# Kernel tuning notes

Hardware: AMD Instinct MI355X
Metric: run time of the kernel (lower is better)

## Reference

```python
import jax, jax.numpy as jnp
import numpy as np


def _squash(s, axis=-1, eps=1e-8):
    # squash(s) = |s|^2/(1+|s|^2) * s/|s|
    s2 = jnp.sum(s * s, axis=axis, keepdims=True)
    return (s2 / (1.0 + s2)) * s / jnp.sqrt(s2 + eps)


def _conv(x, w, b, stride):
    y = jax.lax.conv_general_dilated(
        x, w, (stride, stride), 'VALID',
        dimension_numbers=('NCHW', 'OIHW', 'NCHW'))
    return y + b[None, :, None, None]


def setup_inputs() -> dict:
    key = jax.random.key(0)
    ks = jax.random.split(key, 4)
    B = 64
    sc = 0.05
    return {
        'x': jax.random.normal(ks[0], (B, 3, 32, 32), jnp.float32),
        'conv_w': jax.random.normal(ks[1], (256, 3, 9, 9), jnp.float32) * sc,
        'conv_b': jnp.zeros((256,), jnp.float32),
        'pcap_w': jax.random.normal(ks[2], (256, 256, 9, 9), jnp.float32) * sc,
        'pcap_b': jnp.zeros((256,), jnp.float32),
        'W': jax.random.normal(ks[3], (100, 2048, 16, 8), jnp.float32) * sc,
    }


def reference(x, conv_w, conv_b, pcap_w, pcap_b, W):
    # Conv stem: [B,3,32,32] -> [B,256,24,24]
    h = jax.nn.relu(_conv(x, conv_w, conv_b, 1))
    # PrimaryCaps conv: [B,256,24,24] -> [B,256,8,8], then view to capsules
    p = _conv(h, pcap_w, pcap_b, 2)
    u = _squash(p.reshape(p.shape[0], 2048, 8))            # [B,2048,8]
    # DenseCapsule: u_hat[b,o,i,d] = W[o,i,d,k] u[b,i,k]
    u_hat = jnp.einsum('oidk,bik->boid', W, u)             # [B,100,2048,16]
    u_hat_sg = jax.lax.stop_gradient(u_hat)
    b = jnp.zeros(u_hat.shape[:3], u_hat.dtype)            # [B,100,2048]
    routings = 3
    v = None
    for i in range(routings):
        c = jax.nn.softmax(b, axis=1)                      # over out caps
        uh = u_hat if i == routings - 1 else u_hat_sg
        v = _squash(jnp.einsum('boi,boid->bod', c, uh))    # [B,100,16]
        if i < routings - 1:
            b = b + jnp.einsum('bod,boid->boi', v, u_hat_sg)
    return v
```

## Files before the change

### kernel.cpp

```cpp
#include <hip/hip_runtime.h>

#define NB 64
#define NO 100
#define NI 2048
#define ND 16
#define NK 8

#define WS_H    0
#define WS_U    9437184
#define WS_BB   10485760
#define WS_CB   23592960
#define WS_SP   36700160
#define WS_V    38338560
#define WS_PP   WS_BB

typedef __attribute__((ext_vector_type(8))) short bf16x8;
typedef __attribute__((ext_vector_type(16))) float f32x16;
typedef __attribute__((ext_vector_type(4))) float f32x4;

__device__ inline unsigned short f2bf(float x) {
    union { float f; unsigned u; } v; v.f = x;
    unsigned r = (v.u + 0x7FFFu + ((v.u >> 16) & 1u)) >> 16;
    return (unsigned short)r;
}
__device__ inline float bf2f(unsigned short h) {
    union { unsigned u; float f; } v; v.u = ((unsigned)h) << 16;
    return v.f;
}

__global__ __launch_bounds__(256) void conv1_kernel(const float* __restrict__ x,
        const float* __restrict__ w, const float* __restrict__ bias,
        unsigned short* __restrict__ h_hi, unsigned short* __restrict__ h_lo) {
    const int b = blockIdx.x;
    const int ocg = blockIdx.y;
    __shared__ float xl[3 * 32 * 32];
    __shared__ float wl[16 * 243];
    const int tid = threadIdx.x;
    for (int idx = tid; idx < 3072; idx += 256) xl[idx] = x[b * 3072 + idx];
    for (int idx = tid; idx < 16 * 243; idx += 256)
        wl[idx] = w[ocg * 16 * 243 + idx];
    __syncthreads();
    const int lane = tid & 63;
    const int wg = tid >> 6;
    float acc[4][9];
    #pragma unroll
    for (int jj = 0; jj < 4; ++jj) {
        float bv = bias[ocg * 16 + wg * 4 + jj];
        #pragma unroll
        for (int j = 0; j < 9; ++j) acc[jj][j] = bv;
    }
    int xbase[9];
    #pragma unroll
    for (int j = 0; j < 9; ++j) {
        int p = lane + 64 * j;
        xbase[j] = (p / 24) * 32 + (p % 24);
    }
    for (int ic = 0; ic < 3; ++ic)
        for (int ky = 0; ky < 9; ++ky) {
            #pragma unroll
            for (int kx = 0; kx < 9; ++kx) {
                float wv[4];
                #pragma unroll
                for (int jj = 0; jj < 4; ++jj)
                    wv[jj] = wl[(wg * 4 + jj) * 243 + ic * 81 + ky * 9 + kx];
                #pragma unroll
                for (int j = 0; j < 9; ++j) {
                    float xv = xl[ic * 1024 + xbase[j] + ky * 32 + kx];
                    #pragma unroll
                    for (int jj = 0; jj < 4; ++jj)
                        acc[jj][j] = fmaf(xv, wv[jj], acc[jj][j]);
                }
            }
        }
    #pragma unroll
    for (int jj = 0; jj < 4; ++jj) {
        int oc = ocg * 16 + wg * 4 + jj;
        #pragma unroll
        for (int j = 0; j < 9; ++j) {
            int p = lane + 64 * j;
            float v = fmaxf(acc[jj][j], 0.f);
            unsigned short hi = f2bf(v);
            unsigned short lo = f2bf(v - bf2f(hi));
            size_t o = (size_t)(b * 256 + oc) * 576 + p;
            h_hi[o] = hi;
            h_lo[o] = lo;
        }
    }
}

__global__ __launch_bounds__(256) void wb_precompute_kernel(const float* __restrict__ w,
        unsigned short* __restrict__ wBhi, unsigned short* __restrict__ wBlo) {
    const int ic = blockIdx.x;
    const int ocq = blockIdx.y;
    __shared__ float tl[64][85];
    const int tid = threadIdx.x;
    for (int f = tid; f < 5184; f += 256) {
        int oc = f / 81, kk = f % 81;
        tl[oc][kk] = w[(size_t)(ocq * 64 + oc) * 20736 + ic * 81 + kk];
    }
    __syncthreads();
    for (int idx = tid; idx < 9216; idx += 256) {
        int ky = idx >> 10;
        int rem = idx & 1023;
        int ocl = rem >> 4;
        int kx = rem & 15;
        float val = (kx < 9) ? tl[ocl][ky * 9 + kx] : 0.f;
        unsigned short hi = f2bf(val);
        unsigned short lo = f2bf(val - bf2f(hi));
        size_t dst = ((size_t)(ic * 9 + ky) * 256 + ocq * 64 + ocl) * 16 + kx;
        wBhi[dst] = hi;
        wBlo[dst] = lo;
    }
}

__global__ __launch_bounds__(256) void conv2_mfma_kernel(
        const unsigned short* __restrict__ h_hi, const unsigned short* __restrict__ h_lo,
        const unsigned short* __restrict__ wBhi, const unsigned short* __restrict__ wBlo,
        float* __restrict__ pp) {
    const int bpair = blockIdx.x;
    const int ocb = blockIdx.y;
    const int ks = blockIdx.z;
    __shared__ __align__(16) unsigned short Bh[2][128 * 16];
    __shared__ __align__(16) unsigned short Bl[2][128 * 16];
    const int tid = threadIdx.x;
    const int lane = tid & 63;
    const int wid = tid >> 6;
    const int wr = wid >> 1, wc = wid & 1;
    const int l31 = lane & 31, kh = lane >> 5;
    const int slot = tid & 127;
    const int role = tid >> 7;
    const int oy = (slot >> 3) & 7;
    const int ox = slot & 7;
    const unsigned short* hsel = role ? h_lo : h_hi;
    const size_t hrow0 = ((size_t)(bpair * 2 + (slot >> 6)) * 256) * 576;
    const int ic0 = ks * 32;

    const int aoff0 = (wr * 64 + l31) * 16 + kh * 8;
    const int aoff1 = aoff0 + 512;
    const int boff0 = (wc * 64 + l31) * 16 + kh * 8;
    const int boff1 = boff0 + 512;

    f32x16 acc[2][2];
    #pragma unroll
    for (int m = 0; m < 2; ++m)
        #pragma unroll
        for (int n = 0; n < 2; ++n)
            #pragma unroll
            for (int r = 0; r < 16; ++r) acc[m][n][r] = 0.f;

    unsigned int d0, d1, d2, d3, d4;

#define GLOADB(c) { const int ic_ = ic0 + (c) / 9, ky_ = (c) % 9;                          \
    const unsigned int* hp_ = (const unsigned int*)(hsel + hrow0 + (size_t)ic_ * 576       \
        + (2 * oy + ky_) * 24 + 2 * ox);                                                   \
    d0 = hp_[0]; d1 = hp_[1]; d2 = hp_[2]; d3 = hp_[3]; d4 = hp_[4]; }
#define STOREB(buf) { unsigned short* Bdst_ = (role ? Bl[buf] : Bh[buf]) + slot * 16;      \
    uint4 w0_; w0_.x = d0; w0_.y = d1; w0_.z = d2; w0_.w = d3;                             \
    uint4 w1_; w1_.x = d4 & 0xFFFFu; w1_.y = 0u; w1_.z = 0u; w1_.w = 0u;                   \
    *(uint4*)Bdst_ = w0_; *(uint4*)(Bdst_ + 8) = w1_; }
#define LOADA(c, AH, AL) { const int ic_ = ic0 + (c) / 9, ky_ = (c) % 9;                   \
    const size_t base_ = (size_t)ic_ * 36864 + (size_t)ky_ * 4096 + ocb * 2048;            \
    AH[0] = *(const bf16x8*)(wBhi + base_ + aoff0);                                        \
    AH[1] = *(const bf16x8*)(wBhi + base_ + aoff1);                                        \
    AL[0] = *(const bf16x8*)(wBlo + base_ + aoff0);                                        \
    AL[1] = *(const bf16x8*)(wBlo + base_ + aoff1); }
#define MFMA12(AH, AL, buf) {                                                              \
    bf16x8 bh0 = *(const bf16x8*)&Bh[buf][boff0];                                          \
    bf16x8 bh1 = *(const bf16x8*)&Bh[buf][boff1];                                          \
    bf16x8 bl0 = *(const bf16x8*)&Bl[buf][boff0];                                          \
    bf16x8 bl1 = *(const bf16x8*)&Bl[buf][boff1];                                          \
    acc[0][0] = __builtin_amdgcn_mfma_f32_32x32x16_bf16(AH[0], bh0, acc[0][0], 0, 0, 0);   \
    acc[0][0] = __builtin_amdgcn_mfma_f32_32x32x16_bf16(AH[0], bl0, acc[0][0], 0, 0, 0);   \
    acc[0][0] = __builtin_amdgcn_mfma_f32_32x32x16_bf16(AL[0], bh0, acc[0][0], 0, 0, 0);   \
    acc[0][1] = __builtin_amdgcn_mfma_f32_32x32x16_bf16(AH[0], bh1, acc[0][1], 0, 0, 0);   \
    acc[0][1] = __builtin_amdgcn_mfma_f32_32x32x16_bf16(AH[0], bl1, acc[0][1], 0, 0, 0);   \
    acc[0][1] = __builtin_amdgcn_mfma_f32_32x32x16_bf16(AL[0], bh1, acc[0][1], 0, 0, 0);   \
    acc[1][0] = __builtin_amdgcn_mfma_f32_32x32x16_bf16(AH[1], bh0, acc[1][0], 0, 0, 0);   \
    acc[1][0] = __builtin_amdgcn_mfma_f32_32x32x16_bf16(AH[1], bl0, acc[1][0], 0, 0, 0);   \
    acc[1][0] = __builtin_amdgcn_mfma_f32_32x32x16_bf16(AL[1], bh0, acc[1][0], 0, 0, 0);   \
    acc[1][1] = __builtin_amdgcn_mfma_f32_32x32x16_bf16(AH[1], bh1, acc[1][1], 0, 0, 0);   \
    acc[1][1] = __builtin_amdgcn_mfma_f32_32x32x16_bf16(AH[1], bl1, acc[1][1], 0, 0, 0);   \
    acc[1][1] = __builtin_amdgcn_mfma_f32_32x32x16_bf16(AL[1], bh1, acc[1][1], 0, 0, 0); }

    bf16x8 a0h[2], a0l[2], a1h[2], a1l[2];
    GLOADB(0); STOREB(0);
    GLOADB(1);
    LOADA(0, a0h, a0l);
    __syncthreads();
    #pragma unroll 1
    for (int c = 0; c < 288; c += 2) {
        LOADA(c + 1, a1h, a1l);
        MFMA12(a0h, a0l, 0);
        STOREB(1);
        if (c + 2 < 288) GLOADB(c + 2);
        __syncthreads();
        if (c + 2 < 288) LOADA(c + 2, a0h, a0l);
        MFMA12(a1h, a1l, 1);
        if (c + 2 < 288) {
            STOREB(0);
            GLOADB(c + 3);
        }
        __syncthreads();
    }
#undef GLOADB
#undef STOREB
#undef LOADA
#undef MFMA12

    const int b = bpair * 2 + ((wc * 64 + l31) >> 6);
    #pragma unroll
    for (int m = 0; m < 2; ++m)
        #pragma unroll
        for (int n = 0; n < 2; ++n) {
            const int slotg = wc * 64 + n * 32 + l31;
            const int bb = bpair * 2 + (slotg >> 6);
            const int pos = slotg & 63;
            #pragma unroll
            for (int r = 0; r < 16; ++r) {
                const int row = (r & 3) + 8 * (r >> 2) + 4 * kh;
                const int oc = ocb * 128 + wr * 64 + m * 32 + row;
                pp[(((size_t)ks * 64 + bb) * 256 + oc) * 64 + pos] = acc[m][n][r];
            }
        }
    (void)b;
}

__global__ __launch_bounds__(256) void reduce_bias_squash_kernel(
        const float* __restrict__ pp, const float* __restrict__ bias,
        float* __restrict__ u) {
    const int cap = blockIdx.x * 256 + threadIdx.x;
    const int b = cap >> 11;
    const int rem = cap & 2047;
    const int oc = rem >> 3;
    const int oy = rem & 7;
    float4 sa = {0.f, 0.f, 0.f, 0.f}, sb = {0.f, 0.f, 0.f, 0.f};
    #pragma unroll
    for (int ks = 0; ks < 8; ++ks) {
        const float4* p4 = (const float4*)&pp[(((size_t)ks * 64 + b) * 256 + oc) * 64 + oy * 8];
        float4 a = p4[0], c = p4[1];
        sa.x += a.x; sa.y += a.y; sa.z += a.z; sa.w += a.w;
        sb.x += c.x; sb.y += c.y; sb.z += c.z; sb.w += c.w;
    }
    const float bv = bias[oc];
    sa.x += bv; sa.y += bv; sa.z += bv; sa.w += bv;
    sb.x += bv; sb.y += bv; sb.z += bv; sb.w += bv;
    float s2 = sa.x * sa.x + sa.y * sa.y + sa.z * sa.z + sa.w * sa.w
             + sb.x * sb.x + sb.y * sb.y + sb.z * sb.z + sb.w * sb.w;
    float scale = (s2 / (1.f + s2)) / sqrtf(s2 + 1e-8f);
    sa.x *= scale; sa.y *= scale; sa.z *= scale; sa.w *= scale;
    sb.x *= scale; sb.y *= scale; sb.z *= scale; sb.w *= scale;
    float4* up = (float4*)&u[(size_t)cap * 8];
    up[0] = sa;
    up[1] = sb;
}

__global__ __launch_bounds__(256) void transpose_u_kernel(const float* __restrict__ u,
        float* __restrict__ ut) {
    const int blk = blockIdx.x;
    __shared__ float tl[64 * 132];
    const int tid = threadIdx.x;
    #pragma unroll
    for (int rep = 0; rep < 8; ++rep) {
        const int idx = tid + 256 * rep;
        const int b = idx >> 5, q = idx & 31;
        float4 uv = *(const float4*)(u + (size_t)b * 16384 + blk * 128 + 4 * q);
        *(float4*)&tl[b * 132 + 4 * q] = uv;
    }
    __syncthreads();
    #pragma unroll
    for (int rep = 0; rep < 32; ++rep) {
        const int row = rep * 4 + (tid >> 6);
        const int b = tid & 63;
        ut[(size_t)(blk * 128 + row) * 64 + b] = tl[b * 132 + row];
    }
}

template <int UNIFORM>
__global__ __launch_bounds__(256) void r_weighted_mfma_kernel(
        const float* __restrict__ W, const float* __restrict__ u,
        const float* __restrict__ cbuf, float* __restrict__ sp) {
    const int o = blockIdx.x;
    const int st = blockIdx.y;
    __shared__ __align__(16) unsigned short Ahi[16 * 72];
    __shared__ __align__(16) unsigned short Alo[16 * 72];
    __shared__ __align__(16) unsigned short Bhi[64 * 72];
    __shared__ __align__(16) unsigned short Blo[64 * 72];
    const int tid = threadIdx.x;
    const int lane = tid & 63;
    const int w = tid >> 6;
    const int l15 = lane & 15;
    const int hi = lane >> 4;
    const int sb = tid >> 2;
    const int si = tid & 3;
    f32x4 acc = {0.f, 0.f, 0.f, 0.f};
    const float* Wo = W + (size_t)o * 262144;
    const int i_base = st * 256;
    #pragma unroll 1
    for (int iter = 0; iter < 32; ++iter) {
        const int i0 = i_base + iter * 8;
        __syncthreads();
        {
            float4 wv = *(const float4*)(Wo + (size_t)i0 * 128 + 4 * tid);
            const int i_l = tid >> 5;
            const int d = (tid >> 1) & 15;
            const int k0 = (tid & 1) * 4;
            unsigned short* dh = Ahi + d * 72 + i_l * 8 + k0;
            unsigned short* dl = Alo + d * 72 + i_l * 8 + k0;
            float vv[4] = {wv.x, wv.y, wv.z, wv.w};
            unsigned int h01, h23, l01, l23;
            unsigned short h, l;
            h = f2bf(vv[0]); l = f2bf(vv[0] - bf2f(h)); h01 = h; l01 = l;
            h = f2bf(vv[1]); l = f2bf(vv[1] - bf2f(h)); h01 |= (unsigned)h << 16; l01 |= (unsigned)l << 16;
            h = f2bf(vv[2]); l = f2bf(vv[2] - bf2f(h)); h23 = h; l23 = l;
            h = f2bf(vv[3]); l = f2bf(vv[3] - bf2f(h)); h23 |= (unsigned)h << 16; l23 |= (unsigned)l << 16;
            *(unsigned int*)dh = h01; *(unsigned int*)(dh + 2) = h23;
            *(unsigned int*)dl = l01; *(unsigned int*)(dl + 2) = l23;
        }
        #pragma unroll
        for (int half = 0; half < 2; ++half) {
            const int i_l = si + 4 * half;
            const float* up = u + (size_t)sb * 16384 + (size_t)(i0 + i_l) * 8;
            float4 u0 = *(const float4*)up;
            float4 u1 = *(const float4*)(up + 4);
            float cv = UNIFORM ? 0.01f
                               : cbuf[(size_t)sb * (NO * NI) + o * NI + i0 + i_l];
            float q[8] = {u0.x * cv, u0.y * cv, u0.z * cv, u0.w * cv,
                          u1.x * cv, u1.y * cv, u1.z * cv, u1.w * cv};
            uint4 ph, pl;
            unsigned short h0, h1, l0, l1;
            h0 = f2bf(q[0]); l0 = f2bf(q[0] - bf2f(h0));
            h1 = f2bf(q[1]); l1 = f2bf(q[1] - bf2f(h1));
            ph.x = h0 | ((unsigned)h1 << 16); pl.x = l0 | ((unsigned)l1 << 16);
            h0 = f2bf(q[2]); l0 = f2bf(q[2] - bf2f(h0));
            h1 = f2bf(q[3]); l1 = f2bf(q[3] - bf2f(h1));
            ph.y = h0 | ((unsigned)h1 << 16); pl.y = l0 | ((unsigned)l1 << 16);
            h0 = f2bf(q[4]); l0 = f2bf(q[4] - bf2f(h0));
            h1 = f2bf(q[5]); l1 = f2bf(q[5] - bf2f(h1));
            ph.z = h0 | ((unsigned)h1 << 16); pl.z = l0 | ((unsigned)l1 << 16);
            h0 = f2bf(q[6]); l0 = f2bf(q[6] - bf2f(h0));
            h1 = f2bf(q[7]); l1 = f2bf(q[7] - bf2f(h1));
            ph.w = h0 | ((unsigned)h1 << 16); pl.w = l0 | ((unsigned)l1 << 16);
            *(uint4*)(Bhi + sb * 72 + i_l * 8) = ph;
            *(uint4*)(Blo + sb * 72 + i_l * 8) = pl;
        }
        __syncthreads();
        #pragma unroll
        for (int ch = 0; ch < 2; ++ch) {
            bf16x8 ah = *(const bf16x8*)(Ahi + l15 * 72 + ch * 32 + hi * 8);
            bf16x8 al = *(const bf16x8*)(Alo + l15 * 72 + ch * 32 + hi * 8);
            bf16x8 bh = *(const bf16x8*)(Bhi + (w * 16 + l15) * 72 + ch * 32 + hi * 8);
            bf16x8 bl = *(const bf16x8*)(Blo + (w * 16 + l15) * 72 + ch * 32 + hi * 8);
            acc = __builtin_amdgcn_mfma_f32_16x16x32_bf16(ah, bh, acc, 0, 0, 0);
            acc = __builtin_amdgcn_mfma_f32_16x16x32_bf16(ah, bl, acc, 0, 0, 0);
            acc = __builtin_amdgcn_mfma_f32_16x16x32_bf16(al, bh, acc, 0, 0, 0);
        }
    }
    const int bg = w * 16 + l15;
    float4 st4;
    st4.x = acc[0]; st4.y = acc[1]; st4.z = acc[2]; st4.w = acc[3];
    *(float4*)&sp[(((size_t)o * 8 + st) * 64 + bg) * 16 + hi * 4] = st4;
}

__global__ __launch_bounds__(256) void squash_v_kernel(const float* __restrict__ sp,
        float* __restrict__ dest) {
    const int t = blockIdx.x * 256 + threadIdx.x;
    const int d = t & 15;
    const int cap = t >> 4;
    const int o = cap >> 6;
    const int bb = cap & 63;
    float s = 0.f;
    #pragma unroll
    for (int st = 0; st < 8; ++st)
        s += sp[(((size_t)o * 8 + st) * 64 + bb) * 16 + d];
    float s2 = s * s;
    #pragma unroll
    for (int off = 1; off < 16; off <<= 1)
        s2 += __shfl_xor(s2, off, 16);
    float scale = (s2 / (1.f + s2)) / sqrtf(s2 + 1e-8f);
    dest[(bb * NO + o) * ND + d] = s * scale;
}

template <int ADD>
__global__ __launch_bounds__(256) void r_logits_mfma_kernel(
        const float* __restrict__ W, const float* __restrict__ ut,
        const float* __restrict__ v, float* __restrict__ bbuf) {
    const int o = blockIdx.x;
    const int st = blockIdx.y;
    __shared__ __align__(16) unsigned short Aext[128 * 40];
    __shared__ __align__(16) unsigned short B1[64 * 40];
    __shared__ __align__(16) unsigned short B2[64 * 40];
    __shared__ float ul[128 * 66];
    const int tid = threadIdx.x;
    const int lane = tid & 63;
    const int w = tid >> 6;
    const int l15 = lane & 15;
    const int hi = lane >> 4;
    const float* Wo = W + (size_t)o * 262144;
    {
        const int b = tid >> 2;
        const int dq = (tid & 3) * 4;
        float4 vv = *(const float4*)&v[((size_t)b * NO + o) * ND + dq];
        float q[4] = {vv.x, vv.y, vv.z, vv.w};
        #pragma unroll
        for (int c = 0; c < 4; ++c) {
            unsigned short h = f2bf(q[c]);
            unsigned short l = f2bf(q[c] - bf2f(h));
            B1[b * 40 + dq + c] = h;
            B1[b * 40 + 16 + dq + c] = h;
            B2[b * 40 + dq + c] = l;
            B2[b * 40 + 16 + dq + c] = 0;
        }
    }
    __syncthreads();
    #pragma unroll 1
    for (int iter = 0; iter < 8; ++iter) {
        __syncthreads();
        #pragma unroll
        for (int rep = 0; rep < 2; ++rep) {
            const int off = 4 * tid + 1024 * rep;
            float4 wv = *(const float4*)(Wo + (size_t)(st * 128 + iter * 16) * 128 + off);
            const int i_l = off >> 7;
            const int d = (off >> 3) & 15;
            const int k0 = off & 7;
            float va[4] = {wv.x, wv.y, wv.z, wv.w};
            #pragma unroll
            for (int c = 0; c < 4; ++c) {
                unsigned short h = f2bf(va[c]);
                unsigned short l = f2bf(va[c] - bf2f(h));
                const int row = i_l * 8 + k0 + c;
                Aext[row * 40 + d] = h;
                Aext[row * 40 + 16 + d] = l;
            }
        }
        const int base_row = (st * 128 + iter * 16) * 8;
        #pragma unroll
        for (int rep = 0; rep < 8; ++rep) {
            const int idx = tid + 256 * rep;
            const int row = idx >> 4, bq = idx & 15;
            float4 uv = *(const float4*)(ut + (size_t)(base_row + row) * 64 + 4 * bq);
            *(float4*)&ul[row * 66 + 4 * bq] = uv;
        }
        __syncthreads();
        f32x4 acc[8];
        bf16x8 bf1 = *(const bf16x8*)&B1[(w * 16 + l15) * 40 + hi * 8];
        bf16x8 bf2 = *(const bf16x8*)&B2[(w * 16 + l15) * 40 + hi * 8];
        #pragma unroll
        for (int mt = 0; mt < 8; ++mt) {
            f32x4 z = {0.f, 0.f, 0.f, 0.f};
            bf16x8 af = *(const bf16x8*)&Aext[(mt * 16 + l15) * 40 + hi * 8];
            z = __builtin_amdgcn_mfma_f32_16x16x32_bf16(af, bf1, z, 0, 0, 0);
            z = __builtin_amdgcn_mfma_f32_16x16x32_bf16(af, bf2, z, 0, 0, 0);
            acc[mt] = z;
        }
        #pragma unroll
        for (int mt = 0; mt < 8; ++mt) {
            float partial = 0.f;
            #pragma unroll
            for (int r = 0; r < 4; ++r) {
                const int grow = mt * 16 + hi * 4 + r;
                partial = fmaf(acc[mt][r], ul[grow * 66 + w * 16 + l15], partial);
            }
            float sum = partial + __shfl_xor(partial, 16);
            if ((hi & 1) == 0) {
                const int i_glob = st * 128 + iter * 16 + mt * 2 + (hi >> 1);
                const int bg = w * 16 + l15;
                const size_t addr = (size_t)bg * (NO * NI) + (size_t)o * NI + i_glob;
                bbuf[addr] = (ADD ? bbuf[addr] : 0.f) + sum;
            }
        }
    }
}

__global__ __launch_bounds__(256) void softmax_kernel(const float* __restrict__ bbuf,
        float* __restrict__ cbuf) {
    const int bb = blockIdx.x >> 3;
    const int i = (blockIdx.x & 7) * 256 + threadIdx.x;
    const float* col = bbuf + bb * (NO * NI) + i;
    float m = -1e30f;
    for (int o = 0; o < NO; ++o) m = fmaxf(m, col[o * NI]);
    float s = 0.f;
    for (int o = 0; o < NO; ++o) s += __expf(col[o * NI] - m);
    const float inv = 1.f / s;
    float* outp = cbuf + bb * (NO * NI) + i;
    for (int o = 0; o < NO; ++o) outp[o * NI] = __expf(col[o * NI] - m) * inv;
}

extern "C" void kernel_launch(void* const* d_in, const int* in_sizes, int n_in,
                              void* d_out, int out_size, void* d_ws, size_t ws_size,
                              hipStream_t stream) {
    (void)in_sizes; (void)n_in; (void)out_size; (void)ws_size;
    const float* x      = (const float*)d_in[0];
    const float* conv_w = (const float*)d_in[1];
    const float* conv_b = (const float*)d_in[2];
    const float* pcap_w = (const float*)d_in[3];
    const float* pcap_b = (const float*)d_in[4];
    const float* W      = (const float*)d_in[5];
    float* out = (float*)d_out;
    float* ws  = (float*)d_ws;
    unsigned short* h_hi = (unsigned short*)(ws + WS_H);
    unsigned short* h_lo = h_hi + 9437184;
    unsigned short* wBhi = (unsigned short*)(ws + WS_CB);
    unsigned short* wBlo = wBhi + 9437184;
    float* ut  = ws + WS_H;
    float* u   = ws + WS_U;
    float* bbf = ws + WS_BB;
    float* cbf = ws + WS_CB;
    float* sp  = ws + WS_SP;
    float* v   = ws + WS_V;
    float* pp  = ws + WS_PP;

    wb_precompute_kernel<<<dim3(256, 4), 256, 0, stream>>>(pcap_w, wBhi, wBlo);
    conv1_kernel<<<dim3(64, 16), 256, 0, stream>>>(x, conv_w, conv_b, h_hi, h_lo);
    conv2_mfma_kernel<<<dim3(32, 2, 8), 256, 0, stream>>>(h_hi, h_lo, wBhi, wBlo, pp);
    reduce_bias_squash_kernel<<<512, 256, 0, stream>>>(pp, pcap_b, u);
    transpose_u_kernel<<<128, 256, 0, stream>>>(u, ut);
    r_weighted_mfma_kernel<1><<<dim3(100, 8), 256, 0, stream>>>(W, u, nullptr, sp);
    squash_v_kernel<<<400, 256, 0, stream>>>(sp, v);
    r_logits_mfma_kernel<0><<<dim3(100, 16), 256, 0, stream>>>(W, ut, v, bbf);
    softmax_kernel<<<512, 256, 0, stream>>>(bbf, cbf);
    r_weighted_mfma_kernel<0><<<dim3(100, 8), 256, 0, stream>>>(W, u, cbf, sp);
    squash_v_kernel<<<400, 256, 0, stream>>>(sp, v);
    r_logits_mfma_kernel<1><<<dim3(100, 16), 256, 0, stream>>>(W, ut, v, bbf);
    softmax_kernel<<<512, 256, 0, stream>>>(bbf, cbf);
    r_weighted_mfma_kernel<0><<<dim3(100, 8), 256, 0, stream>>>(W, u, cbf, sp);
    squash_v_kernel<<<400, 256, 0, stream>>>(sp, out);
}
```

Baseline: 850.8 us.

## Pad conv2 LDS B tile rows and simplify double-buffer pipeline

Pads each B-tile row in shared memory from 16 to 20 bf16 elements to reduce LDS bank conflicts on the MFMA operand reads, switching the reads and writes to 8-byte accesses. The main loop also becomes a single-step double buffer: the next global B load is issued, the A weights for the current step are loaded directly, and then the MFMAs run. This removes the A-register prefetch one step ahead, so weight-load latency may be less hidden, and narrower LDS accesses add instruction count.

```diff
diff --git a/kernel.cpp b/kernel.cpp
--- a/kernel.cpp
+++ b/kernel.cpp
@@ -120,8 +120,8 @@
     const int bpair = blockIdx.x;
     const int ocb = blockIdx.y;
     const int ks = blockIdx.z;
-    __shared__ __align__(16) unsigned short Bh[2][128 * 16];
-    __shared__ __align__(16) unsigned short Bl[2][128 * 16];
+    __shared__ __align__(16) unsigned short Bh[2][128 * 20];
+    __shared__ __align__(16) unsigned short Bl[2][128 * 20];
     const int tid = threadIdx.x;
     const int lane = tid & 63;
     const int wid = tid >> 6;
@@ -134,11 +134,9 @@
     const unsigned short* hsel = role ? h_lo : h_hi;
     const size_t hrow0 = ((size_t)(bpair * 2 + (slot >> 6)) * 256) * 576;
     const int ic0 = ks * 32;
-
-    const int aoff0 = (wr * 64 + l31) * 16 + kh * 8;
-    const int aoff1 = aoff0 + 512;
-    const int boff0 = (wc * 64 + l31) * 16 + kh * 8;
-    const int boff1 = boff0 + 512;
+    const size_t abase = (size_t)ocb * 2048 + (size_t)(wr * 64 + l31) * 16 + kh * 8;
+    const int boff0 = (wc * 64 + l31) * 20 + kh * 8;
+    const int boff1 = boff0 + 32 * 20;
 
     f32x16 acc[2][2];
     #pragma unroll
@@ -149,65 +147,63 @@
             for (int r = 0; r < 16; ++r) acc[m][n][r] = 0.f;
 
     unsigned int d0, d1, d2, d3, d4;
+    bf16x8 ah0, ah1, al0, al1;
 
 #define GLOADB(c) { const int ic_ = ic0 + (c) / 9, ky_ = (c) % 9;                          \
     const unsigned int* hp_ = (const unsigned int*)(hsel + hrow0 + (size_t)ic_ * 576       \
         + (2 * oy + ky_) * 24 + 2 * ox);                                                   \
     d0 = hp_[0]; d1 = hp_[1]; d2 = hp_[2]; d3 = hp_[3]; d4 = hp_[4]; }
-#define STOREB(buf) { unsigned short* Bdst_ = (role ? Bl[buf] : Bh[buf]) + slot * 16;      \
-    uint4 w0_; w0_.x = d0; w0_.y = d1; w0_.z = d2; w0_.w = d3;                             \
-    uint4 w1_; w1_.x = d4 & 0xFFFFu; w1_.y = 0u; w1_.z = 0u; w1_.w = 0u;                   \
-    *(uint4*)Bdst_ = w0_; *(uint4*)(Bdst_ + 8) = w1_; }
-#define LOADA(c, AH, AL) { const int ic_ = ic0 + (c) / 9, ky_ = (c) % 9;                   \
-    const size_t base_ = (size_t)ic_ * 36864 + (size_t)ky_ * 4096 + ocb * 2048;            \
-    AH[0] = *(const bf16x8*)(wBhi + base_ + aoff0);                                        \
-    AH[1] = *(const bf16x8*)(wBhi + base_ + aoff1);                                        \
-    AL[0] = *(const bf16x8*)(wBlo + base_ + aoff0);                                        \
-    AL[1] = *(const bf16x8*)(wBlo + base_ + aoff1); }
-#define MFMA12(AH, AL, buf) {                                                              \
-    bf16x8 bh0 = *(const bf16x8*)&Bh[buf][boff0];                                          \
-    bf16x8 bh1 = *(const bf16x8*)&Bh[buf][boff1];                                          \
-    bf16x8 bl0 = *(const bf16x8*)&Bl[buf][boff0];                                          \
-    bf16x8 bl1 = *(const bf16x8*)&Bl[buf][boff1];                                          \
-    acc[0][0] = __builtin_amdgcn_mfma_f32_32x32x16_bf16(AH[0], bh0, acc[0][0], 0, 0, 0);   \
-    acc[0][0] = __builtin_amdgcn_mfma_f32_32x32x16_bf16(AH[0], bl0, acc[0][0], 0, 0, 0);   \
-    acc[0][0] = __builtin_amdgcn_mfma_f32_32x32x16_bf16(AL[0], bh0, acc[0][0], 0, 0, 0);   \
-    acc[0][1] = __builtin_amdgcn_mfma_f32_32x32x16_bf16(AH[0], bh1, acc[0][1], 0, 0, 0);   \
-    acc[0][1] = __builtin_amdgcn_mfma_f32_32x32x16_bf16(AH[0], bl1, acc[0][1], 0, 0, 0);   \
-    acc[0][1] = __builtin_amdgcn_mfma_f32_32x32x16_bf16(AL[0], bh1, acc[0][1], 0, 0, 0);   \
-    acc[1][0] = __builtin_amdgcn_mfma_f32_32x32x16_bf16(AH[1], bh0, acc[1][0], 0, 0, 0);   \
-    acc[1][0] = __builtin_amdgcn_mfma_f32_32x32x16_bf16(AH[1], bl0, acc[1][0], 0, 0, 0);   \
-    acc[1][0] = __builtin_amdgcn_mfma_f32_32x32x16_bf16(AL[1], bh0, acc[1][0], 0, 0, 0);   \
-    acc[1][1] = __builtin_amdgcn_mfma_f32_32x32x16_bf16(AH[1], bh1, acc[1][1], 0, 0, 0);   \
-    acc[1][1] = __builtin_amdgcn_mfma_f32_32x32x16_bf16(AH[1], bl1, acc[1][1], 0, 0, 0);   \
-    acc[1][1] = __builtin_amdgcn_mfma_f32_32x32x16_bf16(AL[1], bh1, acc[1][1], 0, 0, 0); }
-
-    bf16x8 a0h[2], a0l[2], a1h[2], a1l[2];
-    GLOADB(0); STOREB(0);
-    GLOADB(1);
-    LOADA(0, a0h, a0l);
+#define STOREB(buf) { unsigned short* Bdst_ = (role ? Bl[buf] : Bh[buf]) + slot * 20;      \
+    uint2 p0_; p0_.x = d0; p0_.y = d1;                                                     \
+    uint2 p1_; p1_.x = d2; p1_.y = d3;                                                     \
+    uint2 p2_; p2_.x = d4 & 0xFFFFu; p2_.y = 0u;                                           \
+    uint2 p3_; p3_.x = 0u; p3_.y = 0u;                                                     \
+    *(uint2*)(Bdst_) = p0_; *(uint2*)(Bdst_ + 4) = p1_;                                    \
+    *(uint2*)(Bdst_ + 8) = p2_; *(uint2*)(Bdst_ + 12) = p3_; }
+#define LOADA(c) { const int ic_ = ic0 + (c) / 9, ky_ = (c) % 9;                           \
+    const size_t base_ = (size_t)ic_ * 36864 + (size_t)ky_ * 4096 + abase;                 \
+    ah0 = *(const bf16x8*)(wBhi + base_);                                                  \
+    ah1 = *(const bf16x8*)(wBhi + base_ + 512);                                            \
+    al0 = *(const bf16x8*)(wBlo + base_);                                                  \
+    al1 = *(const bf16x8*)(wBlo + base_ + 512); }
+#define LDSB(arr, off, dst) { union { struct { uint2 a, b; } p; bf16x8 v; } u_;            \
+    u_.p.a = *(const uint2*)((arr) + (off));                                               \
+    u_.p.b = *(const uint2*)((arr) + (off) + 4);                                           \
+    dst = u_.v; }
+#define MFMA12(buf) { bf16x8 bh0, bh1, bl0, bl1;                                           \
+    LDSB(Bh[buf], boff0, bh0); LDSB(Bh[buf], boff1, bh1);                                  \
+    LDSB(Bl[buf], boff0, bl0); LDSB(Bl[buf], boff1, bl1);                                  \
+    acc[0][0] = __builtin_amdgcn_mfma_f32_32x32x16_bf16(ah0, bh0, acc[0][0], 0, 0, 0);     \
+    acc[0][0] = __builtin_amdgcn_mfma_f32_32x32x16_bf16(ah0, bl0, acc[0][0], 0, 0, 0);     \
+    acc[0][0] = __builtin_amdgcn_mfma_f32_32x32x16_bf16(al0, bh0, acc[0][0], 0, 0, 0);     \
+    acc[0][1] = __builtin_amdgcn_mfma_f32_32x32x16_bf16(ah0, bh1, acc[0][1], 0, 0, 0);     \
+    acc[0][1] = __builtin_amdgcn_mfma_f32_32x32x16_bf16(ah0, bl1, acc[0][1], 0, 0, 0);     \
+    acc[0][1] = __builtin_amdgcn_mfma_f32_32x32x16_bf16(al0, bh1, acc[0][1], 0, 0, 0);     \
+    acc[1][0] = __builtin_amdgcn_mfma_f32_32x32x16_bf16(ah1, bh0, acc[1][0], 0, 0, 0);     \
+    acc[1][0] = __builtin_amdgcn_mfma_f32_32x32x16_bf16(ah1, bl0, acc[1][0], 0, 0, 0);     \
+    acc[1][0] = __builtin_amdgcn_mfma_f32_32x32x16_bf16(al1, bh0, acc[1][0], 0, 0, 0);     \
+    acc[1][1] = __builtin_amdgcn_mfma_f32_32x32x16_bf16(ah1, bh1, acc[1][1], 0, 0, 0);     \
+    acc[1][1] = __builtin_amdgcn_mfma_f32_32x32x16_bf16(ah1, bl1, acc[1][1], 0, 0, 0);     \
+    acc[1][1] = __builtin_amdgcn_mfma_f32_32x32x16_bf16(al1, bh1, acc[1][1], 0, 0, 0); }
+
+    GLOADB(0);
+    STOREB(0);
     __syncthreads();
     #pragma unroll 1
-    for (int c = 0; c < 288; c += 2) {
-        LOADA(c + 1, a1h, a1l);
-        MFMA12(a0h, a0l, 0);
-        STOREB(1);
-        if (c + 2 < 288) GLOADB(c + 2);
-        __syncthreads();
-        if (c + 2 < 288) LOADA(c + 2, a0h, a0l);
-        MFMA12(a1h, a1l, 1);
-        if (c + 2 < 288) {
-            STOREB(0);
-            GLOADB(c + 3);
-        }
+    for (int c = 0; c < 288; ++c) {
+        const int cur = c & 1;
+        if (c < 287) GLOADB(c + 1);
+        LOADA(c);
+        MFMA12(cur);
+        if (c < 287) STOREB(cur ^ 1);
         __syncthreads();
     }
 #undef GLOADB
 #undef STOREB
 #undef LOADA
+#undef LDSB
 #undef MFMA12
 
-    const int b = bpair * 2 + ((wc * 64 + l31) >> 6);
     #pragma unroll
     for (int m = 0; m < 2; ++m)
         #pragma unroll
@@ -222,7 +218,6 @@
                 pp[(((size_t)ks * 64 + bb) * 256 + oc) * 64 + pos] = acc[m][n][r];
             }
         }
-    (void)b;
 }
 
 __global__ __launch_bounds__(256) void reduce_bias_squash_kernel(
```

Result: slower. 974.3 us (+14.5%).
